# Optimization experiments

Measured on AMD Instinct MI355X. Metric: run time of the kernel, lower is better.

## Reference

```python
import jax, jax.numpy as jnp
import numpy as np

B, Cfi, H, W = 2, 32, 192, 192
Cfp, Cfo, NUM = 1, 2, 16
N = H * W
Ct = Cfo + Cfi + Cfi + Cfp  # 67
EPS = 1e-5


def _bn(x, g, b, m, v):
    # x: (B, C, num, N); per-channel inference batchnorm
    inv = g * jax.lax.rsqrt(v + EPS)
    return x * inv[None, :, None, None] + (b - m * inv)[None, :, None, None]


def _pconv(x, Wt):
    # 1x1 conv as channel contraction: Wt (Cout, Cin), x (B, Cin, num, N)
    return jnp.einsum('oc,bcmn->bomn', Wt, x)


def setup_inputs() -> dict:
    key = jax.random.key(0)
    ks = jax.random.split(key, 32)
    inp = {
        'If': jax.random.normal(ks[0], (B, Cfi, H, W), jnp.float32),
        'Pf': jax.random.normal(ks[1], (B, Cfp, H, W), jnp.float32),
        'Ofnum': jax.random.normal(ks[2], (B, Cfo, NUM, N), jnp.float32),
        'args': jax.random.randint(ks[3], (B, NUM, N), 0, N, jnp.int64),
    }
    def conv_w(k, co, ci):
        return jax.random.normal(k, (co, ci), jnp.float32) * (1.0 / np.sqrt(ci))
    def bn_p(k, c):
        k1, k2 = jax.random.split(k)
        return (jnp.ones((c,), jnp.float32),
                jnp.zeros((c,), jnp.float32),
                jax.random.normal(k1, (c,), jnp.float32) * 0.1,
                jax.random.uniform(k2, (c,), jnp.float32, 0.5, 1.5))
    # convXF: Ct->Cfi, Cfi->Cfi (both BN+GELU)
    inp['W1'] = conv_w(ks[4], Cfi, Ct)
    inp['g1'], inp['b1'], inp['m1'], inp['v1'] = bn_p(ks[5], Cfi)
    inp['W2'] = conv_w(ks[6], Cfi, Cfi)
    inp['g2'], inp['b2'], inp['m2'], inp['v2'] = bn_p(ks[7], Cfi)
    # convXL: Cfi->Cfi (BN+GELU), Cfi->Cfi (BN only)
    inp['W3'] = conv_w(ks[8], Cfi, Cfi)
    inp['g3'], inp['b3'], inp['m3'], inp['v3'] = bn_p(ks[9], Cfi)
    inp['W4'] = conv_w(ks[10], Cfi, Cfi)
    inp['g4'], inp['b4'], inp['m4'], inp['v4'] = bn_p(ks[11], Cfi)
    # coef: Cfi -> 3, with bias
    inp['Wc'] = conv_w(ks[12], 3, Cfi)
    inp['bc'] = jax.random.normal(ks[13], (3,), jnp.float32) * 0.01
    return inp


def reference(If, Pf, Ofnum, args,
              W1, g1, b1, m1, v1,
              W2, g2, b2, m2, v2,
              W3, g3, b3, m3, v3,
              W4, g4, b4, m4, v4,
              Wc, bc):
    gelu = lambda x: jax.nn.gelu(x, approximate=False)
    If_flat = If.reshape(B, Cfi, N)   # (B, Cfi, N)
    Pf_flat = Pf.reshape(B, Cfp, N)   # (B, Cfp, M), M == N here

    # per-batch neighbor gather along flattened spatial dim
    gath = jax.vmap(lambda f, a: f[:, a])  # (C,N),(num,N) -> (C,num,N)
    IPfnum = gath(If_flat, args)            # (B, Cfi, num, N)
    Pfnum = gath(Pf_flat, args)             # (B, Cfp, num, N)
    Ifnum = jnp.broadcast_to(If_flat[:, :, None, :], (B, Cfi, NUM, N))

    X = jnp.concatenate([Ifnum, IPfnum, Pfnum, Ofnum], axis=1)  # (B, Ct, num, N)

    h = gelu(_bn(_pconv(X, W1), g1, b1, m1, v1))
    h = gelu(_bn(_pconv(h, W2), g2, b2, m2, v2))
    l = gelu(_bn(_pconv(h, W3), g3, b3, m3, v3))
    l = _bn(_pconv(l, W4), g4, b4, m4, v4)
    XF = gelu(h + l)

    feat = _pconv(XF, Wc) + bc[None, :, None, None]  # (B, 3, num, N)
    Alpha, Beta, Omega = feat[:, 0:1], feat[:, 1:2], feat[:, 2:3]
    Omega = jax.nn.softmax(Omega, axis=2)
    dout = jnp.sum(((Alpha + 1.0) * Pfnum[:, -1:] + Beta) * Omega,
                   axis=2, keepdims=True)  # (B, 1, 1, N)
    return dout.reshape(B, 1, H, W)
```

## Files before the change

### kernel.cpp

```cpp
#include <hip/hip_runtime.h>
#include <math.h>

#define BB   2
#define CFI  32
#define NN   36864
#define NUMM 16

#define ZOFS (BB * NN * CFI)

typedef __attribute__((ext_vector_type(8))) short short8;
typedef __attribute__((ext_vector_type(4))) float f4;
typedef __attribute__((ext_vector_type(16))) float f16v;

static __device__ __forceinline__ f16v mm32(short8 a, short8 b, f16v c) {
    return __builtin_amdgcn_mfma_f32_32x32x16_bf16(a, b, c, 0, 0, 0);
}

static __device__ __forceinline__ float gelu_fast(float x) {
    const float x2  = x * x;
    const float q   = fmaf(-0.10294310f, x2, -2.30211813f);
    const float e   = exp2f(q * x);
    const float r   = __builtin_amdgcn_rcpf(e + 1.0f);
    return x * r;
}

static __device__ __forceinline__ unsigned bf16_rne_bits(float x) {
    unsigned u = __builtin_bit_cast(unsigned, x);
    return u + 0x7fffu + ((u >> 16) & 1u);
}
static __device__ __forceinline__ void split_pack(float x0, float x1,
                                                  unsigned& hi, unsigned& lo) {
    unsigned r0 = bf16_rne_bits(x0);
    unsigned r1 = bf16_rne_bits(x1);
    float h0 = __builtin_bit_cast(float, r0 & 0xffff0000u);
    float h1 = __builtin_bit_cast(float, r1 & 0xffff0000u);
    hi = (r0 >> 16) | (r1 & 0xffff0000u);
    unsigned s0 = bf16_rne_bits(x0 - h0);
    unsigned s1 = bf16_rne_bits(x1 - h1);
    lo = (s0 >> 16) | (s1 & 0xffff0000u);
}

static __device__ __forceinline__ unsigned pack2(float a, float b) {
    unsigned ua = __builtin_bit_cast(unsigned, a) + 0x8000u;
    unsigned ub = __builtin_bit_cast(unsigned, b) + 0x8000u;
    return (ua >> 16) | (ub & 0xffff0000u);
}

union UV { unsigned u[4]; short8 v; };

__global__ __launch_bounds__(256) void yz_kernel(
    const float* __restrict__ If, const float* __restrict__ Pf,
    const float* __restrict__ W1, const float* __restrict__ g1,
    const float* __restrict__ b1, const float* __restrict__ m1,
    const float* __restrict__ v1,
    float* __restrict__ wsYZ)
{
    __shared__ float wy[1024], wz[1024], wp[32], bt1[32];
    for (int i = threadIdx.x; i < 1024; i += 256) {
        int o = i >> 5, c = i & 31;
        float inv = g1[o] * rsqrtf(v1[o] + 1e-5f);
        wy[i] = W1[o * 67 + c]      * inv;
        wz[i] = W1[o * 67 + 32 + c] * inv;
    }
    if (threadIdx.x < 32) {
        int o = threadIdx.x;
        float inv = g1[o] * rsqrtf(v1[o] + 1e-5f);
        wp[o]  = W1[o * 67 + 64] * inv;
        bt1[o] = b1[o] - m1[o] * inv;
    }
    __syncthreads();

    const int r  = threadIdx.x & 3;
    const int p  = blockIdx.x * 64 + (threadIdx.x >> 2);
    const int b  = p / NN, n = p - b * NN;
    const int o0 = r * 8;
    const float* ifp = If + (size_t)b * CFI * NN + n;

    float v[32];
#pragma unroll
    for (int c = 0; c < 32; c++) v[c] = ifp[(size_t)c * NN];
    const float pf = Pf[p];

    float accY[8], accZ[8];
#pragma unroll
    for (int j = 0; j < 8; j++) {
        const float4* wyr = (const float4*)&wy[(o0 + j) * 32];
        const float4* wzr = (const float4*)&wz[(o0 + j) * 32];
        float ay = bt1[o0 + j];
        float az = wp[o0 + j] * pf;
#pragma unroll
        for (int c4 = 0; c4 < 8; c4++) {
            float4 a = wyr[c4], z = wzr[c4];
            ay = fmaf(a.x, v[4 * c4 + 0], ay);  az = fmaf(z.x, v[4 * c4 + 0], az);
            ay = fmaf(a.y, v[4 * c4 + 1], ay);  az = fmaf(z.y, v[4 * c4 + 1], az);
            ay = fmaf(a.z, v[4 * c4 + 2], ay);  az = fmaf(z.z, v[4 * c4 + 2], az);
            ay = fmaf(a.w, v[4 * c4 + 3], ay);  az = fmaf(z.w, v[4 * c4 + 3], az);
        }
        accY[j] = ay; accZ[j] = az;
    }

    float4* yp = (float4*)(wsYZ + (size_t)p * 32 + o0);
    float4* zp = (float4*)(wsYZ + ZOFS + (size_t)p * 32 + o0);
    yp[0] = make_float4(accY[0], accY[1], accY[2], accY[3]);
    yp[1] = make_float4(accY[4], accY[5], accY[6], accY[7]);
    zp[0] = make_float4(accZ[0], accZ[1], accZ[2], accZ[3]);
    zp[1] = make_float4(accZ[4], accZ[5], accZ[6], accZ[7]);
}

#define LAYER(Lc, BIN0, BIN1, ACCV)                                           \
    {                                                                         \
        const f4 bq0 = *(const f4*)&btl[(Lc) * 32 +      4 * hi + 4 * io];    \
        const f4 bq1 = *(const f4*)&btl[(Lc) * 32 +  8 + 4 * hi + 4 * io];    \
        const f4 bq2 = *(const f4*)&btl[(Lc) * 32 + 16 + 4 * hi + 4 * io];    \
        const f4 bq3 = *(const f4*)&btl[(Lc) * 32 + 24 + 4 * hi + 4 * io];    \
        ACCV[0]  = bq0[0]; ACCV[1]  = bq0[1]; ACCV[2]  = bq0[2]; ACCV[3]  = bq0[3]; \
        ACCV[4]  = bq1[0]; ACCV[5]  = bq1[1]; ACCV[6]  = bq1[2]; ACCV[7]  = bq1[3]; \
        ACCV[8]  = bq2[0]; ACCV[9]  = bq2[1]; ACCV[10] = bq2[2]; ACCV[11] = bq2[3]; \
        ACCV[12] = bq3[0]; ACCV[13] = bq3[1]; ACCV[14] = bq3[2]; ACCV[15] = bq3[3]; \
        short8 Af;                                                            \
        Af = *(const short8*)&wfrag[(Lc)][0][1][lane + io][0];                \
        ACCV = mm32(Af, BIN0.v, ACCV);                                        \
        Af = *(const short8*)&wfrag[(Lc)][0][0][lane + io][0];                \
        ACCV = mm32(Af, BIN0.v, ACCV);                                        \
        Af = *(const short8*)&wfrag[(Lc)][1][1][lane + io][0];                \
        ACCV = mm32(Af, BIN1.v, ACCV);                                        \
        Af = *(const short8*)&wfrag[(Lc)][1][0][lane + io][0];                \
        ACCV = mm32(Af, BIN1.v, ACCV);                                        \
    }

#define RELAYOUT(SRC, B0V, B1V)                                               \
    {                                                                         \
        B0V.u[0] = pack2(SRC[0],  SRC[1]);                                    \
        B0V.u[1] = pack2(SRC[2],  SRC[3]);                                    \
        B0V.u[2] = pack2(SRC[4],  SRC[5]);                                    \
        B0V.u[3] = pack2(SRC[6],  SRC[7]);                                    \
        B1V.u[0] = pack2(SRC[8],  SRC[9]);                                    \
        B1V.u[1] = pack2(SRC[10], SRC[11]);                                   \
        B1V.u[2] = pack2(SRC[12], SRC[13]);                                   \
        B1V.u[3] = pack2(SRC[14], SRC[15]);                                   \
    }

__global__ __launch_bounds__(256, 4) void main_kernel(
    const float* __restrict__ Pf, const float* __restrict__ Of,
    const int* __restrict__ args,
    const float* __restrict__ W1, const float* __restrict__ g1,
    const float* __restrict__ v1,
    const float* __restrict__ W2, const float* __restrict__ g2,
    const float* __restrict__ b2, const float* __restrict__ m2,
    const float* __restrict__ v2,
    const float* __restrict__ W3, const float* __restrict__ g3,
    const float* __restrict__ b3, const float* __restrict__ m3,
    const float* __restrict__ v3,
    const float* __restrict__ W4, const float* __restrict__ g4,
    const float* __restrict__ b4, const float* __restrict__ m4,
    const float* __restrict__ v4,
    const float* __restrict__ Wc, const float* __restrict__ bc,
    const float* __restrict__ ws, float* __restrict__ out)
{
    __shared__ __align__(16) unsigned wfrag[3][2][2][64][4];
    __shared__ __align__(16) float btl[3 * 32];
    __shared__ __align__(16) float wch[3 * 32];
    __shared__ __align__(16) float w1t[2 * 32];
    __shared__ float bcs[3];
    __shared__ int   izs;

    const float* Ws[3] = {W2, W3, W4};
    const float* gs[3] = {g2, g3, g4};
    const float* vs[3] = {v2, v3, v4};
    const float* bs[3] = {b2, b3, b4};
    const float* ms[3] = {m2, m3, m4};

    for (int idx = threadIdx.x; idx < 1536; idx += 256) {
        int pp  = idx & 3;
        int ln  = (idx >> 2) & 63;
        int kh  = (idx >> 8) & 1;
        int L   = idx >> 9;
        int row = ln & 31;
        int g   = ln >> 5;
        int k   = kh * 16 + 4 * g + 2 * (pp & 1) + 8 * (pp >> 1);
        float inv = gs[L][row] * rsqrtf(vs[L][row] + 1e-5f);
        float w0 = Ws[L][row * 32 + k]     * inv;
        float w1 = Ws[L][row * 32 + k + 1] * inv;
        unsigned hiw, low;
        split_pack(w0, w1, hiw, low);
        wfrag[L][kh][0][ln][pp] = hiw;
        wfrag[L][kh][1][ln][pp] = low;
    }
    if (threadIdx.x < 96) {
        int L = threadIdx.x >> 5, ch = threadIdx.x & 31;
        btl[threadIdx.x] = bs[L][ch] - ms[L][ch] * (gs[L][ch] * rsqrtf(vs[L][ch] + 1e-5f));
        wch[threadIdx.x] = Wc[L * 32 + ch];
    }
    if (threadIdx.x < 64) {
        int t = threadIdx.x >> 5, ch = threadIdx.x & 31;
        float i1 = g1[ch] * rsqrtf(v1[ch] + 1e-5f);
        w1t[threadIdx.x] = W1[ch * 67 + 65 + t] * i1;
    }
    if (threadIdx.x < 3) bcs[threadIdx.x] = bc[threadIdx.x];
    if (threadIdx.x == 0) izs = (int)(args[0] >> 16);
    __syncthreads();

    const int lane  = threadIdx.x & 63;
    const int wid   = threadIdx.x >> 6;
    const int m     = lane & 15;
    const int pt    = (lane >> 4) & 1;
    const int hi    = lane >> 5;
    const int q4    = hi << 2;
    const int izero = izs;

#pragma unroll 1
    for (int i = 0; i < 2; i++) {
        const int io = i & izero;
        const int C  = blockIdx.x * 16 + wid * 4 + i * 2 + pt;
        const int b  = (C >= NN) ? 1 : 0;
        const int n  = C - b * NN;

        const int   aIdx = args[(b * NUMM + m) * NN + n];
        const float of0v = Of[((b * 2 + 0) * NUMM + m) * NN + n];
        const float of1v = Of[((b * 2 + 1) * NUMM + m) * NN + n];
        const float pfg  = Pf[b * NN + aIdx];

        const f4* yb = (const f4*)(ws + (size_t)(b * NN + n) * 32);
        const f4* zb = (const f4*)(ws + ZOFS + (size_t)(b * NN + aIdx) * 32);
        f4 y0 = yb[hi], y1 = yb[2 + hi], y2 = yb[4 + hi], y3 = yb[6 + hi];
        f4 z0 = zb[hi], z1 = zb[2 + hi], z2 = zb[4 + hi], z3 = zb[6 + hi];

        const f4 wa0 = *(const f4*)&w1t[q4 + 4 * io];
        const f4 wa1 = *(const f4*)&w1t[8 + q4 + 4 * io];
        const f4 wa2 = *(const f4*)&w1t[16 + q4 + 4 * io];
        const f4 wa3 = *(const f4*)&w1t[24 + q4 + 4 * io];
        const f4 wb0 = *(const f4*)&w1t[32 + q4 + 4 * io];
        const f4 wb1 = *(const f4*)&w1t[40 + q4 + 4 * io];
        const f4 wb2 = *(const f4*)&w1t[48 + q4 + 4 * io];
        const f4 wb3 = *(const f4*)&w1t[56 + q4 + 4 * io];

        float x[16];
#pragma unroll
        for (int j = 0; j < 4; j++) {
            x[j]      = fmaf(of1v, wb0[j], fmaf(of0v, wa0[j], y0[j] + z0[j]));
            x[4 + j]  = fmaf(of1v, wb1[j], fmaf(of0v, wa1[j], y1[j] + z1[j]));
            x[8 + j]  = fmaf(of1v, wb2[j], fmaf(of0v, wa2[j], y2[j] + z2[j]));
            x[12 + j] = fmaf(of1v, wb3[j], fmaf(of0v, wa3[j], y3[j] + z3[j]));
        }
#pragma unroll
        for (int j = 0; j < 16; j++) x[j] = gelu_fast(x[j]);
        UV B0, B1;
        RELAYOUT(x, B0, B1);

        f16v acc;
        LAYER(0, B0, B1, acc);
        float h2g[16];
#pragma unroll
        for (int r = 0; r < 16; r++) h2g[r] = gelu_fast(acc[r]);
        RELAYOUT(h2g, B0, B1);

        LAYER(1, B0, B1, acc);
        float h3g[16];
#pragma unroll
        for (int r = 0; r < 16; r++) h3g[r] = gelu_fast(acc[r]);
        RELAYOUT(h3g, B0, B1);

        LAYER(2, B0, B1, acc);

        float pa = 0.0f, pb = 0.0f, po = 0.0f;
#pragma unroll
        for (int q = 0; q < 4; q++) {
            const f4 wAq = *(const f4*)&wch[      8 * q + q4 + 4 * io];
            const f4 wBq = *(const f4*)&wch[32 +  8 * q + q4 + 4 * io];
            const f4 wOq = *(const f4*)&wch[64 +  8 * q + q4 + 4 * io];
#pragma unroll
            for (int r2 = 0; r2 < 4; r2++) {
                float xf = gelu_fast(h2g[4 * q + r2] + acc[4 * q + r2]);
                pa = fmaf(wAq[r2], xf, pa);
                pb = fmaf(wBq[r2], xf, pb);
                po = fmaf(wOq[r2], xf, po);
            }
        }
        pa += __shfl_xor(pa, 32, 64);
        pb += __shfl_xor(pb, 32, 64);
        po += __shfl_xor(po, 32, 64);

        const float alpha = pa + bcs[0];
        const float beta_ = pb + bcs[1];
        const float omega = po + bcs[2];
        const float val = fmaf(alpha + 1.0f, pfg, beta_);

        float mx = omega;
#pragma unroll
        for (int s = 1; s < 16; s <<= 1) mx = fmaxf(mx, __shfl_xor(mx, s, 64));
        const float e = __expf(omega - mx);
        float S = e, T = val * e;
#pragma unroll
        for (int s = 1; s < 16; s <<= 1) {
            S += __shfl_xor(S, s, 64);
            T += __shfl_xor(T, s, 64);
        }
        if ((lane & 15) == 0 && lane < 32)
            out[b * NN + n] = T * __builtin_amdgcn_rcpf(S);
    }
}

extern "C" void kernel_launch(void* const* d_in, const int* in_sizes, int n_in,
                              void* d_out, int out_size, void* d_ws, size_t ws_size,
                              hipStream_t stream) {
    const float* If    = (const float*)d_in[0];
    const float* Pf    = (const float*)d_in[1];
    const float* Of    = (const float*)d_in[2];
    const int*   args  = (const int*)d_in[3];
    const float* W1    = (const float*)d_in[4];
    const float* g1    = (const float*)d_in[5];
    const float* b1    = (const float*)d_in[6];
    const float* m1    = (const float*)d_in[7];
    const float* v1    = (const float*)d_in[8];
    const float* W2    = (const float*)d_in[9];
    const float* g2    = (const float*)d_in[10];
    const float* b2    = (const float*)d_in[11];
    const float* m2    = (const float*)d_in[12];
    const float* v2    = (const float*)d_in[13];
    const float* W3    = (const float*)d_in[14];
    const float* g3    = (const float*)d_in[15];
    const float* b3    = (const float*)d_in[16];
    const float* m3    = (const float*)d_in[17];
    const float* v3    = (const float*)d_in[18];
    const float* W4    = (const float*)d_in[19];
    const float* g4    = (const float*)d_in[20];
    const float* b4    = (const float*)d_in[21];
    const float* m4    = (const float*)d_in[22];
    const float* v4    = (const float*)d_in[23];
    const float* Wc    = (const float*)d_in[24];
    const float* bc    = (const float*)d_in[25];

    float* ws  = (float*)d_ws;
    float* out = (float*)d_out;

    yz_kernel<<<(BB * NN) / 64, 256, 0, stream>>>(
        If, Pf, W1, g1, b1, m1, v1, ws);

    main_kernel<<<(BB * NN) / 16, 256, 0, stream>>>(
        Pf, Of, args,
        W1, g1, v1,
        W2, g2, b2, m2, v2,
        W3, g3, b3, m3, v3,
        W4, g4, b4, m4, v4,
        Wc, bc, ws, out);
}
```

Before: 232.9 us.

## Software-pipeline next iteration's gathers behind MFMA layers and double work per block

Each wave now processes four iterations instead of two, with the grid halved. Loads for the next iteration (y rows, Of values, the gathered z rows, Pf, and the index two steps ahead) are issued in the middle of the current iteration's MFMA layers. The goal is to hide global and gather memory latency behind compute. The cost is higher register pressure and fewer blocks, which may lower occupancy.

```diff
diff --git a/kernel.cpp b/kernel.cpp
--- a/kernel.cpp
+++ b/kernel.cpp
@@ -208,22 +208,36 @@
     const int q4    = hi << 2;
     const int izero = izs;
 
+    const int base  = blockIdx.x * 32 + wid * 8 + pt;
+
+    f4 y0, y1, y2, y3, z0, z1, z2, z3;
+    float of0v, of1v, pfg_n;
+    int   aI_n;
+    {
+        const int C0 = base;
+        const int b0 = (C0 >= NN) ? 1 : 0;
+        const int n0 = C0 - b0 * NN;
+        const int a0 = args[(b0 * NUMM + m) * NN + n0];
+        of0v = Of[((b0 * 2 + 0) * NUMM + m) * NN + n0];
+        of1v = Of[((b0 * 2 + 1) * NUMM + m) * NN + n0];
+        pfg_n = Pf[b0 * NN + a0];
+        const f4* yb = (const f4*)(ws + (size_t)(b0 * NN + n0) * 32);
+        const f4* zb = (const f4*)(ws + ZOFS + (size_t)(b0 * NN + a0) * 32);
+        y0 = yb[hi]; y1 = yb[2 + hi]; y2 = yb[4 + hi]; y3 = yb[6 + hi];
+        z0 = zb[hi]; z1 = zb[2 + hi]; z2 = zb[4 + hi]; z3 = zb[6 + hi];
+        const int C1 = (C0 + 2 < BB * NN) ? C0 + 2 : BB * NN - 1;
+        const int b1_ = (C1 >= NN) ? 1 : 0;
+        const int n1_ = C1 - b1_ * NN;
+        aI_n = args[(b1_ * NUMM + m) * NN + n1_];
+    }
+
 #pragma unroll 1
-    for (int i = 0; i < 2; i++) {
+    for (int i = 0; i < 4; i++) {
         const int io = i & izero;
-        const int C  = blockIdx.x * 16 + wid * 4 + i * 2 + pt;
+        const int C  = base + i * 2;
         const int b  = (C >= NN) ? 1 : 0;
         const int n  = C - b * NN;
-
-        const int   aIdx = args[(b * NUMM + m) * NN + n];
-        const float of0v = Of[((b * 2 + 0) * NUMM + m) * NN + n];
-        const float of1v = Of[((b * 2 + 1) * NUMM + m) * NN + n];
-        const float pfg  = Pf[b * NN + aIdx];
-
-        const f4* yb = (const f4*)(ws + (size_t)(b * NN + n) * 32);
-        const f4* zb = (const f4*)(ws + ZOFS + (size_t)(b * NN + aIdx) * 32);
-        f4 y0 = yb[hi], y1 = yb[2 + hi], y2 = yb[4 + hi], y3 = yb[6 + hi];
-        f4 z0 = zb[hi], z1 = zb[2 + hi], z2 = zb[4 + hi], z3 = zb[6 + hi];
+        const float pfg = pfg_n;
 
         const f4 wa0 = *(const f4*)&w1t[q4 + 4 * io];
         const f4 wa1 = *(const f4*)&w1t[8 + q4 + 4 * io];
@@ -247,6 +261,10 @@
         UV B0, B1;
         RELAYOUT(x, B0, B1);
 
+        const int Cn = (C + 2 < BB * NN) ? C + 2 : BB * NN - 1;
+        const int bn = (Cn >= NN) ? 1 : 0;
+        const int nn = Cn - bn * NN;
+
         f16v acc;
         LAYER(0, B0, B1, acc);
         float h2g[16];
@@ -254,11 +272,29 @@
         for (int r = 0; r < 16; r++) h2g[r] = gelu_fast(acc[r]);
         RELAYOUT(h2g, B0, B1);
 
+        {
+            const f4* ybn = (const f4*)(ws + (size_t)(bn * NN + nn) * 32);
+            y0 = ybn[hi]; y1 = ybn[2 + hi]; y2 = ybn[4 + hi]; y3 = ybn[6 + hi];
+            of0v = Of[((bn * 2 + 0) * NUMM + m) * NN + nn];
+            of1v = Of[((bn * 2 + 1) * NUMM + m) * NN + nn];
+        }
+
         LAYER(1, B0, B1, acc);
         float h3g[16];
 #pragma unroll
         for (int r = 0; r < 16; r++) h3g[r] = gelu_fast(acc[r]);
         RELAYOUT(h3g, B0, B1);
+
+        {
+            const int aN = aI_n;
+            pfg_n = Pf[bn * NN + aN];
+            const f4* zbn = (const f4*)(ws + ZOFS + (size_t)(bn * NN + aN) * 32);
+            z0 = zbn[hi]; z1 = zbn[2 + hi]; z2 = zbn[4 + hi]; z3 = zbn[6 + hi];
+            const int Ca = (C + 4 < BB * NN) ? C + 4 : BB * NN - 1;
+            const int ba = (Ca >= NN) ? 1 : 0;
+            const int na = Ca - ba * NN;
+            aI_n = args[(ba * NUMM + m) * NN + na];
+        }
 
         LAYER(2, B0, B1, acc);
 
@@ -336,7 +372,7 @@
     yz_kernel<<<(BB * NN) / 64, 256, 0, stream>>>(
         If, Pf, W1, g1, b1, m1, v1, ws);
 
-    main_kernel<<<(BB * NN) / 16, 256, 0, stream>>>(
+    main_kernel<<<(BB * NN) / 32, 256, 0, stream>>>(
         Pf, Of, args,
         W1, g1, v1,
         W2, g2, b2, m2, v2,
```

New measurement: 227.4 us. 2.4% less time.
